# Performance work log

Measured on AMD Instinct MI355X. Metric: run time of the kernel, lower is better.

## Reference

```python
import jax, jax.numpy as jnp
import numpy as np

N = 20000   # nodes
E = 320000  # edges
F0 = 32     # num_features
H = 8       # GAT heads
G = 64      # graphs in batch


def setup_inputs() -> dict:
    key = jax.random.key(0)
    ks = jax.random.split(key, 16)
    def p(k, shape, s=0.05):
        return jax.random.normal(k, shape, jnp.float32) * s
    d = {}
    d['x'] = jax.random.normal(ks[0], (N, F0), jnp.float32)
    d['edge_index'] = jax.random.randint(ks[1], (2, E), 0, N, dtype=jnp.int32)
    d['edge_weights'] = jax.random.uniform(ks[2], (E,), jnp.float32)
    d['batch'] = jnp.sort(jax.random.randint(ks[3], (N,), 0, G, dtype=jnp.int32))
    # GATConv(32 -> 32, heads=8)
    d['W_gat'] = p(ks[4], (F0, H * F0)); d['att_src'] = p(ks[5], (H, F0))
    d['att_dst'] = p(ks[6], (H, F0));    d['b_gat'] = jnp.zeros((H * F0,), jnp.float32)
    # residual Linear(256 -> 1024) (widened so the residual add is shape-consistent)
    d['W_res'] = p(ks[7], (H * F0, 1024)); d['b_res'] = jnp.zeros((1024,), jnp.float32)
    # GCNConv(256 -> 512) + BN1
    d['W2'] = p(ks[8], (H * F0, 512)); d['b2'] = jnp.zeros((512,), jnp.float32)
    d['g1'] = jnp.ones((512,), jnp.float32); d['be1'] = jnp.zeros((512,), jnp.float32)
    d['m1'] = jnp.zeros((512,), jnp.float32); d['v1'] = jnp.ones((512,), jnp.float32)
    # GCNConv(512 -> 1024) + BN2
    d['W3'] = p(ks[9], (512, 1024)); d['b3'] = jnp.zeros((1024,), jnp.float32)
    d['g2'] = jnp.ones((1024,), jnp.float32); d['be2'] = jnp.zeros((1024,), jnp.float32)
    d['m2'] = jnp.zeros((1024,), jnp.float32); d['v2'] = jnp.ones((1024,), jnp.float32)
    # head
    d['Wf1'] = p(ks[10], (1024, 256)); d['bf1'] = jnp.zeros((256,), jnp.float32)
    d['Wf2'] = p(ks[11], (256, 2));    d['bf2'] = jnp.zeros((2,), jnp.float32)
    return d


def _add_self_loops(edge_index, edge_weight, n):
    loop = jnp.arange(n, dtype=edge_index.dtype)
    ei = jnp.concatenate([edge_index, jnp.stack([loop, loop])], axis=1)
    ew = jnp.concatenate([edge_weight, jnp.ones((n,), edge_weight.dtype)])
    return ei, ew


def _gat(x, edge_index, W, att_src, att_dst, b, n):
    # PyG GATConv, concat=True, eval (attention dropout off). Self-loops already added.
    src, dst = edge_index[0], edge_index[1]
    h = (x @ W).reshape(n, H, -1)                    # [N,H,C]
    a_s = jnp.einsum('nhc,hc->nh', h, att_src)        # [N,H]
    a_d = jnp.einsum('nhc,hc->nh', h, att_dst)
    e = jax.nn.leaky_relu(a_s[src] + a_d[dst], 0.2)   # [E,H]
    m = jax.ops.segment_max(e, dst, num_segments=n)   # softmax over incoming edges
    ex = jnp.exp(e - m[dst])
    s = jax.ops.segment_sum(ex, dst, num_segments=n)
    alpha = ex / s[dst]
    out = jax.ops.segment_sum(h[src] * alpha[:, :, None], dst, num_segments=n)
    return out.reshape(n, -1) + b                     # [N,H*C]


def _gcn(x, edge_index, w, W, b, n):
    # PyG GCNConv with symmetric normalization; self-loops (weight 1) already added.
    src, dst = edge_index[0], edge_index[1]
    deg = jax.ops.segment_sum(w, dst, num_segments=n)
    dinv = jnp.where(deg > 0, jax.lax.rsqrt(jnp.maximum(deg, 1e-12)), 0.0)
    norm = dinv[src] * w * dinv[dst]                  # [E]
    h = x @ W                                         # transform first (cheaper)
    return jax.ops.segment_sum(h[src] * norm[:, None], dst, num_segments=n) + b


def _bn(x, g, b, m, v):
    return g * (x - m) * jax.lax.rsqrt(v + 1e-5) + b


def reference(x, edge_index, edge_weights, batch, W_gat, att_src, att_dst, b_gat,
              W_res, b_res, W2, b2, g1, be1, m1, v1, W3, b3, g2, be2, m2, v2,
              Wf1, bf1, Wf2, bf2):
    n = x.shape[0]
    ei, ew = _add_self_loops(edge_index, edge_weights, n)
    h = jax.nn.relu(_gat(x, ei, W_gat, att_src, att_dst, b_gat, n))   # [N,256]
    res = h @ W_res + b_res                                           # [N,1024]
    h = _gcn(h, ei, ew, W2, b2, n)                                    # [N,512]
    h = jax.nn.relu(_bn(h, g1, be1, m1, v1))
    h = _gcn(h, ei, ew, W3, b3, n)                                    # [N,1024]
    h = jax.nn.relu(_bn(h, g2, be2, m2, v2))
    h = h + res
    pooled = jax.ops.segment_max(h, batch, num_segments=G)            # global max pool [G,1024]
    z = jax.nn.relu(pooled @ Wf1 + bf1)                               # dropout is eval no-op
    return z @ Wf2 + bf2                                              # [G,2]
```

## Files before the change

### kernel.cpp

```cpp
#include <hip/hip_runtime.h>
#include <hip/hip_bf16.h>
#include <hip/hip_fp8.h>

#define NN 20000
#define EE 320000
#define GG 64
#define EN (EE + NN)
#define MT 157
#define SB 79

typedef float f32x4 __attribute__((ext_vector_type(4)));
typedef __bf16 bf16x4 __attribute__((ext_vector_type(4)));
typedef __bf16 bf16x8 __attribute__((ext_vector_type(8)));

__device__ __forceinline__ void gl_lds16(const void* g, void* l) {
    __builtin_amdgcn_global_load_lds((const __attribute__((address_space(1))) void*)g,
                                     (__attribute__((address_space(3))) void*)l, 16, 0, 0);
}

__global__ void sentinel_kernel(float* out, int n) {
    int i = blockIdx.x * 256 + threadIdx.x;
    if (i < n) out[i] = 12345.0f;
}

__global__ __launch_bounds__(256) void front_kernel(
    const float* __restrict__ W2, const float* __restrict__ W3, const float* __restrict__ Wres,
    __bf16* __restrict__ W2t, __bf16* __restrict__ W3t, __bf16* __restrict__ Wrt,
    const float* __restrict__ x, const float* __restrict__ W_gat,
    const float* __restrict__ att_s, const float* __restrict__ att_d,
    float* __restrict__ a_s, float* __restrict__ a_d,
    const int* __restrict__ ei, const float* __restrict__ ew,
    int* deg_cnt, float* deg_w, float* __restrict__ pooled,
    __bf16* __restrict__ xb)
{
    __shared__ float smemf[4160];
    int b = blockIdx.x, tid = threadIdx.x;
    if (b < 224) {
        const float* W; __bf16* Wt; int K, N, bx, by;
        if (b < 32)       { W = W2;   Wt = W2t; K = 256; N = 512;  int bb = b;       bx = bb & 7;  by = bb >> 3; }
        else if (b < 160) { W = W3;   Wt = W3t; K = 512; N = 1024; int bb = b - 32;  bx = bb & 15; by = bb >> 4; }
        else              { W = Wres; Wt = Wrt; K = 256; N = 1024; int bb = b - 160; bx = bb & 15; by = bb >> 4; }
        int kb = by * 64, nb = bx * 64;
        int tx = tid & 63, ty = tid >> 6;
#pragma unroll
        for (int i = ty; i < 64; i += 4)
            smemf[i * 65 + tx] = W[(size_t)(kb + i) * N + nb + tx];
        __syncthreads();
#pragma unroll
        for (int i = ty; i < 64; i += 4)
            Wt[(size_t)(nb + i) * K + kb + tx] = (__bf16)smemf[tx * 65 + i];
    } else if (b < 352) {
        int bb = b - 224;
        float* wss = smemf;
        float* wsd = smemf + 256;
        float* xs  = smemf + 512;
        {
            int h = tid >> 5, k = tid & 31;
            float s = 0.f, d = 0.f;
#pragma unroll
            for (int c = 0; c < 32; c++) {
                float wv = W_gat[k * 256 + h * 32 + c];
                s += wv * att_s[h * 32 + c];
                d += wv * att_d[h * 32 + c];
            }
            wss[h * 32 + k] = s; wsd[h * 32 + k] = d;
        }
        __syncthreads();
        for (int n0 = bb * 32; n0 < NN; n0 += 128 * 32) {
#pragma unroll
            for (int i = 0; i < 4; i++) {
                int idx = tid + i * 256;
                xs[(idx >> 5) * 33 + (idx & 31)] = x[(size_t)n0 * 32 + idx];
            }
            __syncthreads();
            int nl = tid >> 3, h = tid & 7;
            float s = 0.f, d = 0.f;
#pragma unroll
            for (int k = 0; k < 32; k++) {
                float xv = xs[nl * 33 + k];
                s += xv * wss[h * 32 + k];
                d += xv * wsd[h * 32 + k];
            }
            a_s[(n0 + nl) * 8 + h] = s;
            a_d[(n0 + nl) * 8 + h] = d;
            __syncthreads();
        }
    } else if (b < 608) {
        int i = (b - 352) * 256 + tid;
        pooled[i] = -INFINITY;
    } else if (b < 1858) {
        int e = (b - 608) * 256 + tid;
        if (e < EE) {
            int dst = ei[EE + e];
            atomicAdd(&deg_cnt[dst], 1);
            atomicAdd(&deg_w[dst], ew[e]);
        }
    } else {
        int idx0 = (b - 1858) * 2048 + tid * 8;
        if (idx0 < NN * 32) {
            f32x4 a = *(const f32x4*)(x + idx0);
            f32x4 c = *(const f32x4*)(x + idx0 + 4);
            bf16x8 o;
#pragma unroll
            for (int u = 0; u < 4; u++) { o[u] = (__bf16)a[u]; o[u + 4] = (__bf16)c[u]; }
            *(bf16x8*)(xb + idx0) = o;
        }
    }
}

__global__ __launch_bounds__(256) void scan_blocks(const int* __restrict__ deg_cnt, int* __restrict__ bsum) {
    __shared__ int red[256];
    int tid = threadIdx.x, i = blockIdx.x * 256 + tid;
    red[tid] = (i < NN) ? deg_cnt[i] + 1 : 0;
    __syncthreads();
    for (int s = 128; s > 0; s >>= 1) { if (tid < s) red[tid] += red[tid + s]; __syncthreads(); }
    if (tid == 0) bsum[blockIdx.x] = red[0];
}

__global__ __launch_bounds__(256) void scan_write(const int* __restrict__ deg_cnt,
                                                  const int* __restrict__ bsum, int* __restrict__ rowptr) {
    __shared__ int sc[256];
    __shared__ int red[256];
    int tid = threadIdx.x, b = blockIdx.x, i = b * 256 + tid;
    red[tid] = (tid < b && tid < SB) ? bsum[tid] : 0;
    __syncthreads();
    for (int s = 128; s > 0; s >>= 1) { if (tid < s) red[tid] += red[tid + s]; __syncthreads(); }
    int boff = red[0];
    __syncthreads();
    int v = (i < NN) ? deg_cnt[i] + 1 : 0;
    sc[tid] = v;
    __syncthreads();
    for (int ofs = 1; ofs < 256; ofs <<= 1) {
        int t = (tid >= ofs) ? sc[tid - ofs] : 0;
        __syncthreads();
        sc[tid] += t;
        __syncthreads();
    }
    if (i < NN) rowptr[i] = boff + sc[tid] - v;
    if (b == SB - 1 && tid == 255) rowptr[NN] = boff + sc[255];
}

__global__ void fill_kernel(const int* __restrict__ ei, const float* __restrict__ ew,
                            const float* __restrict__ deg_w, const int* __restrict__ rowptr,
                            int* fill, int2* __restrict__ csre) {
    int e = blockIdx.x * 256 + threadIdx.x;
    if (e >= EN) return;
    int src, dst; float w;
    if (e < EE) { src = ei[e]; dst = ei[EE + e]; w = ew[e]; }
    else        { src = dst = e - EE; w = 1.0f; }
    int pos = atomicAdd(&fill[dst], 1);
    int slot = rowptr[dst] + pos;
    float norm = rsqrtf(deg_w[src] + 1.0f) * w * rsqrtf(deg_w[dst] + 1.0f);
    csre[slot] = make_int2(src, __float_as_int(norm));
}

__global__ __launch_bounds__(256) void gat_agg_x(
    const int* __restrict__ rowptr, const int2* __restrict__ csre,
    const float* __restrict__ a_s, const float* __restrict__ a_d,
    const __bf16* __restrict__ xb, __bf16* __restrict__ xagg)
{
    int widx = threadIdx.x >> 6, lane = threadIdx.x & 63;
    int node = blockIdx.x * 4 + widx;
    int base = rowptr[node], deg = rowptr[node + 1] - base;
    int hA = lane & 7, eslot = lane >> 3;
    int c = lane & 31, half = lane >> 5;
    float adA = a_d[node * 8 + hA];
    float acc0[4] = {}, acc1[4] = {}, acc2[4] = {}, acc3[4] = {};

    if (deg <= 64) {
        int sv = (lane < deg) ? csre[base + lane].x : 0;
        float ev[8];
        float psum = 0.f;
#pragma unroll
        for (int j = 0; j < 8; j++) {
            int e = j * 8 + eslot;
            float v = 0.f;
            if (e < deg) {
                int src = __shfl(sv, e);
                float t = a_s[src * 8 + hA] + adA;
                t = (t > 0.f) ? t : 0.2f * t;
                v = __expf(t);
            }
            ev[j] = v;
            psum += v;
        }
#pragma unroll
        for (int m = 8; m <= 32; m <<= 1) psum += __shfl_xor(psum, m);
        float sinv[4];
#pragma unroll
        for (int jj = 0; jj < 4; jj++) sinv[jj] = 1.f / __shfl(psum, half * 4 + jj);
#pragma unroll
        for (int j = 0; j < 8; j++) {
            if (j * 8 >= deg) break;
            int lim = min(8, deg - j * 8);
            int t = 0;
            for (; t + 3 < lim; t += 4) {
                int sA = __shfl(sv, j * 8 + t),     sB = __shfl(sv, j * 8 + t + 1);
                int sC = __shfl(sv, j * 8 + t + 2), sD = __shfl(sv, j * 8 + t + 3);
                float xvA = (float)xb[(size_t)sA * 32 + c];
                float xvB = (float)xb[(size_t)sB * 32 + c];
                float xvC = (float)xb[(size_t)sC * 32 + c];
                float xvD = (float)xb[(size_t)sD * 32 + c];
#pragma unroll
                for (int jj = 0; jj < 4; jj++) {
                    int hb = half * 4 + jj;
                    acc0[jj] += __shfl(ev[j], (t << 3) | hb) * sinv[jj] * xvA;
                    acc1[jj] += __shfl(ev[j], ((t + 1) << 3) | hb) * sinv[jj] * xvB;
                    acc2[jj] += __shfl(ev[j], ((t + 2) << 3) | hb) * sinv[jj] * xvC;
                    acc3[jj] += __shfl(ev[j], ((t + 3) << 3) | hb) * sinv[jj] * xvD;
                }
            }
            for (; t < lim; t++) {
                int src = __shfl(sv, j * 8 + t);
                float xv = (float)xb[(size_t)src * 32 + c];
#pragma unroll
                for (int jj = 0; jj < 4; jj++) {
                    float a = __shfl(ev[j], (t << 3) | (half * 4 + jj)) * sinv[jj];
                    acc0[jj] += a * xv;
                }
            }
        }
    } else {
        float sum = 0.f;
        for (int e = 0; e < deg; e++) {
            int src = csre[base + e].x;
            float t = a_s[src * 8 + hA] + adA;
            t = (t > 0.f) ? t : 0.2f * t;
            sum += __expf(t);
        }
        float sinv[4], ad4[4];
#pragma unroll
        for (int jj = 0; jj < 4; jj++) {
            sinv[jj] = 1.f / __shfl(sum, half * 4 + jj);
            ad4[jj] = a_d[node * 8 + half * 4 + jj];
        }
        for (int e = 0; e < deg; e++) {
            int src = csre[base + e].x;
            float xv = (float)xb[(size_t)src * 32 + c];
#pragma unroll
            for (int jj = 0; jj < 4; jj++) {
                float t = a_s[src * 8 + half * 4 + jj] + ad4[jj];
                t = (t > 0.f) ? t : 0.2f * t;
                acc0[jj] += __expf(t) * sinv[jj] * xv;
            }
        }
    }
#pragma unroll
    for (int jj = 0; jj < 4; jj++)
        xagg[(size_t)node * 256 + (half * 4 + jj) * 32 + c] =
            (__bf16)((acc0[jj] + acc1[jj]) + (acc2[jj] + acc3[jj]));
}

__global__ __launch_bounds__(256) void gat_post(
    const __bf16* __restrict__ xagg, const float* __restrict__ W,
    const float* __restrict__ b_gat, __bf16* __restrict__ h1,
    unsigned char* __restrict__ h1f)
{
    __shared__ float Ws[32 * 256];
    int tid = threadIdx.x;
#pragma unroll
    for (int k = 0; k < 32; k++) Ws[k * 256 + tid] = W[k * 256 + tid];
    float bg = b_gat[tid];
    int lbase = tid & 32;
    __syncthreads();
    for (int n = blockIdx.x; n < NN; n += gridDim.x) {
        float xv = (float)xagg[(size_t)n * 256 + tid];
        float acc = 0.f;
#pragma unroll
        for (int k = 0; k < 32; k++) acc += __shfl(xv, lbase + k) * Ws[k * 256 + tid];
        float v = fmaxf(acc + bg, 0.f);
        h1[(size_t)n * 256 + tid] = (__bf16)v;
        *reinterpret_cast<__hip_fp8_e4m3*>(&h1f[(size_t)n * 256 + tid]) = __hip_fp8_e4m3(16.0f * v);
    }
}

template <int C>
__global__ __launch_bounds__(256) void gcn_agg_fp8(
    const int* __restrict__ rowptr, const int2* __restrict__ csre,
    const unsigned char* __restrict__ feat, __bf16* __restrict__ out)
{
    constexpr int VB = C / 64;
    typedef __bf16 bf16v __attribute__((ext_vector_type(VB)));
    __shared__ float lut[256];
    int tid = threadIdx.x;
    {
        unsigned char bb = (unsigned char)tid;
        __hip_fp8_e4m3 q = *reinterpret_cast<__hip_fp8_e4m3*>(&bb);
        lut[tid] = ((float)q) * 0.0625f;
    }
    __syncthreads();
    int widx = tid >> 6, lane = tid & 63;
    int node = blockIdx.x * 4 + widx;
    int coff = lane * VB;
    int base = rowptr[node], deg = rowptr[node + 1] - base;
    float acc0[VB] = {}, acc1[VB] = {}, acc2[VB] = {}, acc3[VB] = {};
    const unsigned char* fb = feat + coff;
    auto ldv = [&](int src) -> unsigned long long {
        if constexpr (VB == 8) return *(const unsigned long long*)(fb + (size_t)src * C);
        else                   return (unsigned long long)(*(const unsigned int*)(fb + (size_t)src * C));
    };
    for (int e0 = 0; e0 < deg; e0 += 64) {
        int cnt = min(64, deg - e0);
        int sv = 0; float wv = 0.f;
        if (lane < cnt) { int2 m = csre[base + e0 + lane]; sv = m.x; wv = __int_as_float(m.y); }
        int s = 0;
        for (; s + 3 < cnt; s += 4) {
            int sA = __shfl(sv, s),     sB = __shfl(sv, s + 1);
            int sC = __shfl(sv, s + 2), sD = __shfl(sv, s + 3);
            float wA = __shfl(wv, s),     wB = __shfl(wv, s + 1);
            float wC = __shfl(wv, s + 2), wD = __shfl(wv, s + 3);
            unsigned long long vA = ldv(sA), vB = ldv(sB), vC = ldv(sC), vD = ldv(sD);
#pragma unroll
            for (int j = 0; j < VB; j++) {
                acc0[j] += wA * lut[(vA >> (8 * j)) & 0xff];
                acc1[j] += wB * lut[(vB >> (8 * j)) & 0xff];
                acc2[j] += wC * lut[(vC >> (8 * j)) & 0xff];
                acc3[j] += wD * lut[(vD >> (8 * j)) & 0xff];
            }
        }
        for (; s < cnt; s++) {
            int src = __shfl(sv, s);
            float w = __shfl(wv, s);
            unsigned long long v = ldv(src);
#pragma unroll
            for (int j = 0; j < VB; j++) acc0[j] += w * lut[(v >> (8 * j)) & 0xff];
        }
    }
    bf16v o;
#pragma unroll
    for (int j = 0; j < VB; j++) o[j] = (__bf16)((acc0[j] + acc1[j]) + (acc2[j] + acc3[j]));
    *(bf16v*)(out + (size_t)node * C + coff) = o;
}


__device__ __forceinline__ void stage_async64(
    const __bf16* __restrict__ A, int K, const __bf16* __restrict__ Wt,
    int bm, int bn, int k0, int tid, __bf16* As, __bf16* Bs)
{
#pragma unroll
    for (int i = 0; i < 2; i++) {
        int j = i * 512 + tid;
        int r = j >> 3, c = j & 7;
        const __bf16* gp = A + (size_t)(bm + r) * K + k0 + ((c ^ (r & 7)) * 8);
        gl_lds16(gp, As + (size_t)(j & ~63) * 8);
    }
#pragma unroll
    for (int i = 0; i < 2; i++) {
        int j = i * 512 + tid;
        int r = j >> 3, c = j & 7;
        const __bf16* gp = Wt + (size_t)(bn + r) * K + k0 + ((c ^ (r & 7)) * 8);
        gl_lds16(gp, Bs + (size_t)(j & ~63) * 8);
    }
}

__device__ __forceinline__ void mfma_step64(
    const __bf16* As, const __bf16* Bs, int wr, int wc, int l16, int q, f32x4 (&acc)[4][2])
{
#pragma unroll
    for (int ks = 0; ks < 2; ks++) {
        bf16x8 af[4], bfv[2];
#pragma unroll
        for (int mt = 0; mt < 4; mt++) {
            int row = wr * 64 + mt * 16 + l16;
            af[mt] = *(const bf16x8*)(As + row * 64 + (((ks * 4 + q) ^ (row & 7)) * 8));
        }
#pragma unroll
        for (int nt = 0; nt < 2; nt++) {
            int row = wc * 32 + nt * 16 + l16;
            bfv[nt] = *(const bf16x8*)(Bs + row * 64 + (((ks * 4 + q) ^ (row & 7)) * 8));
        }
#pragma unroll
        for (int mt = 0; mt < 4; mt++)
#pragma unroll
            for (int nt = 0; nt < 2; nt++)
                acc[mt][nt] = __builtin_amdgcn_mfma_f32_16x16x32_bf16(af[mt], bfv[nt], acc[mt][nt], 0, 0, 0);
    }
}

__device__ __forceinline__ void gemm_loop(
    const __bf16* __restrict__ A, int K, const __bf16* __restrict__ Wt,
    int bm, int bn, int tid, int wr, int wc, int l16, int q,
    __bf16* As, __bf16* Bs, f32x4 (&acc)[4][2])
{
    for (int k0 = 0; k0 < K; k0 += 64) {
        stage_async64(A, K, Wt, bm, bn, k0, tid, As, Bs);
        __syncthreads();
        mfma_step64(As, Bs, wr, wc, l16, q, acc);
        __syncthreads();
    }
}

__global__ __launch_bounds__(512) void gemm_bn_relu(
    const __bf16* __restrict__ A, const __bf16* __restrict__ Wt,
    int M, int K, int Nc,
    const float* __restrict__ bias,
    const float* __restrict__ g, const float* __restrict__ be,
    const float* __restrict__ mu, const float* __restrict__ var,
    unsigned char* __restrict__ C)
{
    __shared__ __bf16 As[128 * 64];
    __shared__ __bf16 Bs[128 * 64];
    int tid = threadIdx.x;
    int w = tid >> 6, wr = w >> 2, wc = w & 3;
    int l = tid & 63, q = l >> 4, l16 = l & 15;
    int i = blockIdx.x;
    int k = (i & 3) * MT + (i >> 2);
    int bm = (k >> 2) * 128, bn = (k & 3) * 128;
    f32x4 acc[4][2] = {};
    gemm_loop(A, K, Wt, bm, bn, tid, wr, wc, l16, q, As, Bs, acc);
#pragma unroll
    for (int nt = 0; nt < 2; nt++) {
        int gn = bn + wc * 32 + nt * 16 + l16;
        float s = g[gn] * rsqrtf(var[gn] + 1e-5f);
        float t = be[gn] - mu[gn] * s;
        float bv = bias[gn];
#pragma unroll
        for (int mt = 0; mt < 4; mt++)
#pragma unroll
            for (int r = 0; r < 4; r++) {
                int gm = bm + wr * 64 + mt * 16 + q * 4 + r;
                if (gm < M) {
                    float val = fmaxf((acc[mt][nt][r] + bv) * s + t, 0.f);
                    *reinterpret_cast<__hip_fp8_e4m3*>(&C[(size_t)gm * Nc + gn]) =
                        __hip_fp8_e4m3(16.0f * val);
                }
            }
    }
}

__device__ __forceinline__ void atomicMaxFloat(float* addr, float value) {
    if (value >= 0.f) atomicMax((int*)addr, __float_as_int(value));
    else              atomicMin((unsigned int*)addr, __float_as_uint(value));
}

__global__ __launch_bounds__(512) void gemm_final(
    const __bf16* __restrict__ A1, const __bf16* __restrict__ W3t,
    const __bf16* __restrict__ A2, const __bf16* __restrict__ Wrt,
    const float* __restrict__ b3, const float* __restrict__ bres,
    const float* __restrict__ g, const float* __restrict__ be,
    const float* __restrict__ mu, const float* __restrict__ var,
    const int* __restrict__ batch, float* __restrict__ pooled)
{
    const int M = NN;
    __shared__ __bf16 As[128 * 64];
    __shared__ __bf16 Bs[128 * 64];
    __shared__ int bat[128];
    int tid = threadIdx.x;
    int w = tid >> 6, wr = w >> 2, wc = w & 3;
    int l = tid & 63, q = l >> 4, l16 = l & 15;
    int i = blockIdx.x;
    int k = (i & 7) * MT + (i >> 3);
    int bm = (k >> 3) * 128, bn = (k & 7) * 128;
    if (tid < 128) bat[tid] = (bm + tid < M) ? batch[bm + tid] : -1;
    f32x4 acc[4][2] = {};
    f32x4 accR[4][2] = {};
    gemm_loop(A1, 512, W3t, bm, bn, tid, wr, wc, l16, q, As, Bs, acc);
    gemm_loop(A2, 256, Wrt, bm, bn, tid, wr, wc, l16, q, As, Bs, accR);
#pragma unroll
    for (int nt = 0; nt < 2; nt++) {
        int gn = bn + wc * 32 + nt * 16 + l16;
        float s = g[gn] * rsqrtf(var[gn] + 1e-5f);
        float t = be[gn] - mu[gn] * s;
        float bv3 = b3[gn];
        float bvr = bres[gn];
        int cb = -1; float run = 0.f;
#pragma unroll
        for (int mt = 0; mt < 4; mt++)
#pragma unroll
            for (int r = 0; r < 4; r++) {
                int lr = wr * 64 + mt * 16 + q * 4 + r;
                int id = bat[lr];
                if (id < 0) continue;
                float v = fmaxf((acc[mt][nt][r] + bv3) * s + t, 0.f) + accR[mt][nt][r] + bvr;
                if (id == cb) run = fmaxf(run, v);
                else {
                    if (cb >= 0) atomicMaxFloat(&pooled[cb * 1024 + gn], run);
                    cb = id; run = v;
                }
            }
        if (cb >= 0) atomicMaxFloat(&pooled[cb * 1024 + gn], run);
    }
}

__global__ void head_kernel(
    const float* __restrict__ pooled, const float* __restrict__ Wf1, const float* __restrict__ bf1,
    const float* __restrict__ Wf2, const float* __restrict__ bf2, float* __restrict__ out)
{
    int gph = blockIdx.x, tid = threadIdx.x;
    __shared__ float prow[1024];
    __shared__ float zred[256];
    for (int i = tid; i < 1024; i += 256) prow[i] = pooled[gph * 1024 + i];
    __syncthreads();
    float z = 0.f;
    for (int k = 0; k < 1024; k++) z += prow[k] * Wf1[k * 256 + tid];
    z = fmaxf(z + bf1[tid], 0.f);
    for (int c = 0; c < 2; c++) {
        zred[tid] = z * Wf2[tid * 2 + c];
        __syncthreads();
        for (int s = 128; s > 0; s >>= 1) { if (tid < s) zred[tid] += zred[tid + s]; __syncthreads(); }
        if (tid == 0) out[gph * 2 + c] = zred[0] + bf2[c];
        __syncthreads();
    }
}

extern "C" void kernel_launch(void* const* d_in, const int* in_sizes, int n_in,
                              void* d_out, int out_size, void* d_ws, size_t ws_size,
                              hipStream_t stream) {
    const float* x       = (const float*)d_in[0];
    const int*   ei      = (const int*)d_in[1];
    const float* ew      = (const float*)d_in[2];
    const int*   batch   = (const int*)d_in[3];
    const float* W_gat   = (const float*)d_in[4];
    const float* att_src = (const float*)d_in[5];
    const float* att_dst = (const float*)d_in[6];
    const float* b_gat   = (const float*)d_in[7];
    const float* W_res   = (const float*)d_in[8];
    const float* b_res   = (const float*)d_in[9];
    const float* W2      = (const float*)d_in[10];
    const float* b2v     = (const float*)d_in[11];
    const float* g1      = (const float*)d_in[12];
    const float* be1     = (const float*)d_in[13];
    const float* m1      = (const float*)d_in[14];
    const float* v1      = (const float*)d_in[15];
    const float* W3      = (const float*)d_in[16];
    const float* b3      = (const float*)d_in[17];
    const float* g2      = (const float*)d_in[18];
    const float* be2     = (const float*)d_in[19];
    const float* m2      = (const float*)d_in[20];
    const float* v2      = (const float*)d_in[21];
    const float* Wf1     = (const float*)d_in[22];
    const float* bf1     = (const float*)d_in[23];
    const float* Wf2     = (const float*)d_in[24];
    const float* bf2v    = (const float*)d_in[25];
    float* out           = (float*)d_out;

    char* ws = (char*)d_ws;
    size_t off = 0;
    auto alloc = [&](size_t bytes) { size_t o = off; off += (bytes + 255) & ~(size_t)255; return o; };
    size_t o_hlin   = alloc((size_t)NN * 256 * 2);
    size_t o_h1     = alloc((size_t)NN * 256 * 2);
    size_t o_h1f    = alloc((size_t)NN * 256);
    size_t o_h2     = alloc((size_t)NN * 512);
    size_t o_agg2   = alloc((size_t)NN * 512 * 2);
    size_t o_xb     = alloc((size_t)NN * 32 * 2);
    size_t o_as     = alloc((size_t)NN * 8 * 4);
    size_t o_ad     = alloc((size_t)NN * 8 * 4);
    size_t o_degc   = alloc((size_t)NN * 4);
    size_t o_degw   = alloc((size_t)NN * 4);
    size_t o_fill   = alloc((size_t)NN * 4);
    size_t o_rowptr = alloc((size_t)(NN + 1) * 4);
    size_t o_bsum   = alloc((size_t)SB * 4);
    size_t o_csre   = alloc((size_t)EN * 8);
    size_t o_pool   = alloc((size_t)GG * 1024 * 4);
    size_t o_w2t    = alloc((size_t)512 * 256 * 2);
    size_t o_w3t    = alloc((size_t)1024 * 512 * 2);
    size_t o_wrt    = alloc((size_t)1024 * 256 * 2);
    if (off > ws_size) {
        sentinel_kernel<<<(out_size + 255) / 256, 256, 0, stream>>>(out, out_size);
        return;
    }

    __bf16* xagg   = (__bf16*)(ws + o_hlin);
    __bf16* agg1   = xagg;
    __bf16* h1     = (__bf16*)(ws + o_h1);
    unsigned char* h1f = (unsigned char*)(ws + o_h1f);
    unsigned char* h2f = (unsigned char*)(ws + o_h2);
    __bf16* agg2   = (__bf16*)(ws + o_agg2);
    __bf16* xb     = (__bf16*)(ws + o_xb);
    float*  a_s    = (float*)(ws + o_as);
    float*  a_d    = (float*)(ws + o_ad);
    int*    degc   = (int*)(ws + o_degc);
    float*  degw   = (float*)(ws + o_degw);
    int*    fillb  = (int*)(ws + o_fill);
    int*    rowptr = (int*)(ws + o_rowptr);
    int*    bsum   = (int*)(ws + o_bsum);
    int2*   csre   = (int2*)(ws + o_csre);
    float*  pooled = (float*)(ws + o_pool);
    __bf16* W2t    = (__bf16*)(ws + o_w2t);
    __bf16* W3t    = (__bf16*)(ws + o_w3t);
    __bf16* Wrt    = (__bf16*)(ws + o_wrt);

    hipMemsetAsync(ws + o_degc, 0, o_rowptr - o_degc, stream);
    front_kernel<<<2171, 256, 0, stream>>>(W2, W3, W_res, W2t, W3t, Wrt,
        x, W_gat, att_src, att_dst, a_s, a_d, ei, ew, degc, degw, pooled, xb);

    scan_blocks<<<SB, 256, 0, stream>>>(degc, bsum);
    scan_write<<<SB, 256, 0, stream>>>(degc, bsum, rowptr);
    fill_kernel<<<(EN + 255) / 256, 256, 0, stream>>>(ei, ew, degw, rowptr, fillb, csre);

    gat_agg_x<<<NN / 4, 256, 0, stream>>>(rowptr, csre, a_s, a_d, xb, xagg);
    gat_post<<<1280, 256, 0, stream>>>(xagg, W_gat, b_gat, h1, h1f);

    gcn_agg_fp8<256><<<NN / 4, 256, 0, stream>>>(rowptr, csre, h1f, agg1);
    gemm_bn_relu<<<4 * MT, 512, 0, stream>>>(agg1, W2t, NN, 256, 512, b2v,
        g1, be1, m1, v1, h2f);
    gcn_agg_fp8<512><<<NN / 4, 256, 0, stream>>>(rowptr, csre, h2f, agg2);
    gemm_final<<<8 * MT, 512, 0, stream>>>(agg2, W3t, h1, Wrt,
        b3, b_res, g2, be2, m2, v2, batch, pooled);

    head_kernel<<<GG, 256, 0, stream>>>(pooled, Wf1, bf1, Wf2, bf2v, out);
}
```

Before: 376.2 us.

## Pack CSR edges into 32-bit words and process two nodes per wave in GCN aggregation

CSR edge entries are compressed from an int2 (source index plus fp32 norm) to one 32-bit word holding a 16-bit source index and an fp16 norm, halving edge-list traffic. The GCN aggregation kernel now maps half a wave (32 lanes) per node with wider per-lane loads, so each block covers 8 nodes. GAT aggregation pre-scales the attention weights by the softmax denominator once instead of multiplying inside the inner loop. Risks include lower norm precision, a 16-bit source index that relies on N fitting in 65536, and divergence when the two nodes sharing a wave have unequal degree.

```diff
diff --git a/kernel.cpp b/kernel.cpp
--- a/kernel.cpp
+++ b/kernel.cpp
@@ -1,6 +1,7 @@
 #include <hip/hip_runtime.h>
 #include <hip/hip_bf16.h>
 #include <hip/hip_fp8.h>
+#include <hip/hip_fp16.h>
 
 #define NN 20000
 #define EE 320000
@@ -142,7 +143,7 @@
 
 __global__ void fill_kernel(const int* __restrict__ ei, const float* __restrict__ ew,
                             const float* __restrict__ deg_w, const int* __restrict__ rowptr,
-                            int* fill, int2* __restrict__ csre) {
+                            int* fill, unsigned int* __restrict__ csru) {
     int e = blockIdx.x * 256 + threadIdx.x;
     if (e >= EN) return;
     int src, dst; float w;
@@ -151,11 +152,12 @@
     int pos = atomicAdd(&fill[dst], 1);
     int slot = rowptr[dst] + pos;
     float norm = rsqrtf(deg_w[src] + 1.0f) * w * rsqrtf(deg_w[dst] + 1.0f);
-    csre[slot] = make_int2(src, __float_as_int(norm));
+    unsigned short hb = __half_as_ushort(__float2half(norm));
+    csru[slot] = (unsigned int)src | ((unsigned int)hb << 16);
 }
 
 __global__ __launch_bounds__(256) void gat_agg_x(
-    const int* __restrict__ rowptr, const int2* __restrict__ csre,
+    const int* __restrict__ rowptr, const unsigned int* __restrict__ csru,
     const float* __restrict__ a_s, const float* __restrict__ a_d,
     const __bf16* __restrict__ xb, __bf16* __restrict__ xagg)
 {
@@ -168,7 +170,7 @@
     float acc0[4] = {}, acc1[4] = {}, acc2[4] = {}, acc3[4] = {};
 
     if (deg <= 64) {
-        int sv = (lane < deg) ? csre[base + lane].x : 0;
+        int sv = (lane < deg) ? (int)(csru[base + lane] & 0xffffu) : 0;
         float ev[8];
         float psum = 0.f;
 #pragma unroll
@@ -186,9 +188,9 @@
         }
 #pragma unroll
         for (int m = 8; m <= 32; m <<= 1) psum += __shfl_xor(psum, m);
-        float sinv[4];
-#pragma unroll
-        for (int jj = 0; jj < 4; jj++) sinv[jj] = 1.f / __shfl(psum, half * 4 + jj);
+        float sinv_own = 1.f / psum;
+#pragma unroll
+        for (int j = 0; j < 8; j++) ev[j] *= sinv_own;
 #pragma unroll
         for (int j = 0; j < 8; j++) {
             if (j * 8 >= deg) break;
@@ -204,10 +206,10 @@
 #pragma unroll
                 for (int jj = 0; jj < 4; jj++) {
                     int hb = half * 4 + jj;
-                    acc0[jj] += __shfl(ev[j], (t << 3) | hb) * sinv[jj] * xvA;
-                    acc1[jj] += __shfl(ev[j], ((t + 1) << 3) | hb) * sinv[jj] * xvB;
-                    acc2[jj] += __shfl(ev[j], ((t + 2) << 3) | hb) * sinv[jj] * xvC;
-                    acc3[jj] += __shfl(ev[j], ((t + 3) << 3) | hb) * sinv[jj] * xvD;
+                    acc0[jj] += __shfl(ev[j], (t << 3) | hb) * xvA;
+                    acc1[jj] += __shfl(ev[j], ((t + 1) << 3) | hb) * xvB;
+                    acc2[jj] += __shfl(ev[j], ((t + 2) << 3) | hb) * xvC;
+                    acc3[jj] += __shfl(ev[j], ((t + 3) << 3) | hb) * xvD;
                 }
             }
             for (; t < lim; t++) {
@@ -215,7 +217,7 @@
                 float xv = (float)xb[(size_t)src * 32 + c];
 #pragma unroll
                 for (int jj = 0; jj < 4; jj++) {
-                    float a = __shfl(ev[j], (t << 3) | (half * 4 + jj)) * sinv[jj];
+                    float a = __shfl(ev[j], (t << 3) | (half * 4 + jj));
                     acc0[jj] += a * xv;
                 }
             }
@@ -223,7 +225,7 @@
     } else {
         float sum = 0.f;
         for (int e = 0; e < deg; e++) {
-            int src = csre[base + e].x;
+            int src = (int)(csru[base + e] & 0xffffu);
             float t = a_s[src * 8 + hA] + adA;
             t = (t > 0.f) ? t : 0.2f * t;
             sum += __expf(t);
@@ -235,7 +237,7 @@
             ad4[jj] = a_d[node * 8 + half * 4 + jj];
         }
         for (int e = 0; e < deg; e++) {
-            int src = csre[base + e].x;
+            int src = (int)(csru[base + e] & 0xffffu);
             float xv = (float)xb[(size_t)src * 32 + c];
 #pragma unroll
             for (int jj = 0; jj < 4; jj++) {
@@ -276,10 +278,11 @@
 
 template <int C>
 __global__ __launch_bounds__(256) void gcn_agg_fp8(
-    const int* __restrict__ rowptr, const int2* __restrict__ csre,
+    const int* __restrict__ rowptr, const unsigned int* __restrict__ csru,
     const unsigned char* __restrict__ feat, __bf16* __restrict__ out)
 {
-    constexpr int VB = C / 64;
+    constexpr int VB = C / 32;
+    constexpr int NW = VB / 8;
     typedef __bf16 bf16v __attribute__((ext_vector_type(VB)));
     __shared__ float lut[256];
     int tid = threadIdx.x;
@@ -289,47 +292,49 @@
         lut[tid] = ((float)q) * 0.0625f;
     }
     __syncthreads();
-    int widx = tid >> 6, lane = tid & 63;
-    int node = blockIdx.x * 4 + widx;
-    int coff = lane * VB;
+    int wave = tid >> 6, lane = tid & 63;
+    int g = lane >> 5, l = lane & 31, gb = g << 5;
+    int node = blockIdx.x * 8 + wave * 2 + g;
     int base = rowptr[node], deg = rowptr[node + 1] - base;
-    float acc0[VB] = {}, acc1[VB] = {}, acc2[VB] = {}, acc3[VB] = {};
-    const unsigned char* fb = feat + coff;
-    auto ldv = [&](int src) -> unsigned long long {
-        if constexpr (VB == 8) return *(const unsigned long long*)(fb + (size_t)src * C);
-        else                   return (unsigned long long)(*(const unsigned int*)(fb + (size_t)src * C));
+    int degmax = max(deg, __shfl(deg, lane ^ 32));
+    float acc[VB] = {};
+    const unsigned char* fb = feat + l * VB;
+
+    auto ldrow = [&](unsigned int m, unsigned long long* v) {
+        const unsigned char* p = fb + (size_t)(m & 0xffffu) * C;
+        if constexpr (NW == 2) { ulonglong2 t = *(const ulonglong2*)p; v[0] = t.x; v[1] = t.y; }
+        else                   { v[0] = *(const unsigned long long*)p; }
     };
-    for (int e0 = 0; e0 < deg; e0 += 64) {
-        int cnt = min(64, deg - e0);
-        int sv = 0; float wv = 0.f;
-        if (lane < cnt) { int2 m = csre[base + e0 + lane]; sv = m.x; wv = __int_as_float(m.y); }
+    auto accrow = [&](unsigned int m, const unsigned long long* v) {
+        float w = __half2float(__ushort_as_half((unsigned short)(m >> 16)));
+#pragma unroll
+        for (int q = 0; q < NW; q++)
+#pragma unroll
+            for (int j = 0; j < 8; j++)
+                acc[q * 8 + j] += w * lut[(v[q] >> (8 * j)) & 0xff];
+    };
+
+    for (int e0 = 0; e0 < degmax; e0 += 32) {
+        unsigned int mv = (e0 + l < deg) ? csru[base + e0 + l] : 0u;
+        int cnt = min(32, degmax - e0);
         int s = 0;
         for (; s + 3 < cnt; s += 4) {
-            int sA = __shfl(sv, s),     sB = __shfl(sv, s + 1);
-            int sC = __shfl(sv, s + 2), sD = __shfl(sv, s + 3);
-            float wA = __shfl(wv, s),     wB = __shfl(wv, s + 1);
-            float wC = __shfl(wv, s + 2), wD = __shfl(wv, s + 3);
-            unsigned long long vA = ldv(sA), vB = ldv(sB), vC = ldv(sC), vD = ldv(sD);
-#pragma unroll
-            for (int j = 0; j < VB; j++) {
-                acc0[j] += wA * lut[(vA >> (8 * j)) & 0xff];
-                acc1[j] += wB * lut[(vB >> (8 * j)) & 0xff];
-                acc2[j] += wC * lut[(vC >> (8 * j)) & 0xff];
-                acc3[j] += wD * lut[(vD >> (8 * j)) & 0xff];
-            }
+            unsigned int mA = __shfl(mv, gb + s),     mB = __shfl(mv, gb + s + 1);
+            unsigned int mC = __shfl(mv, gb + s + 2), mD = __shfl(mv, gb + s + 3);
+            unsigned long long vA[NW], vB[NW], vC[NW], vD[NW];
+            ldrow(mA, vA); ldrow(mB, vB); ldrow(mC, vC); ldrow(mD, vD);
+            accrow(mA, vA); accrow(mB, vB); accrow(mC, vC); accrow(mD, vD);
         }
         for (; s < cnt; s++) {
-            int src = __shfl(sv, s);
-            float w = __shfl(wv, s);
-            unsigned long long v = ldv(src);
-#pragma unroll
-            for (int j = 0; j < VB; j++) acc0[j] += w * lut[(v >> (8 * j)) & 0xff];
+            unsigned int m = __shfl(mv, gb + s);
+            unsigned long long v[NW];
+            ldrow(m, v); accrow(m, v);
         }
     }
     bf16v o;
 #pragma unroll
-    for (int j = 0; j < VB; j++) o[j] = (__bf16)((acc0[j] + acc1[j]) + (acc2[j] + acc3[j]));
-    *(bf16v*)(out + (size_t)node * C + coff) = o;
+    for (int j = 0; j < VB; j++) o[j] = (__bf16)acc[j];
+    *(bf16v*)(out + (size_t)node * C + l * VB) = o;
 }
 
 
@@ -550,7 +555,7 @@
     size_t o_fill   = alloc((size_t)NN * 4);
     size_t o_rowptr = alloc((size_t)(NN + 1) * 4);
     size_t o_bsum   = alloc((size_t)SB * 4);
-    size_t o_csre   = alloc((size_t)EN * 8);
+    size_t o_csre   = alloc((size_t)EN * 4);
     size_t o_pool   = alloc((size_t)GG * 1024 * 4);
     size_t o_w2t    = alloc((size_t)512 * 256 * 2);
     size_t o_w3t    = alloc((size_t)1024 * 512 * 2);
@@ -574,7 +579,7 @@
     int*    fillb  = (int*)(ws + o_fill);
     int*    rowptr = (int*)(ws + o_rowptr);
     int*    bsum   = (int*)(ws + o_bsum);
-    int2*   csre   = (int2*)(ws + o_csre);
+    unsigned int* csru = (unsigned int*)(ws + o_csre);
     float*  pooled = (float*)(ws + o_pool);
     __bf16* W2t    = (__bf16*)(ws + o_w2t);
     __bf16* W3t    = (__bf16*)(ws + o_w3t);
@@ -586,15 +591,15 @@
 
     scan_blocks<<<SB, 256, 0, stream>>>(degc, bsum);
     scan_write<<<SB, 256, 0, stream>>>(degc, bsum, rowptr);
-    fill_kernel<<<(EN + 255) / 256, 256, 0, stream>>>(ei, ew, degw, rowptr, fillb, csre);
-
-    gat_agg_x<<<NN / 4, 256, 0, stream>>>(rowptr, csre, a_s, a_d, xb, xagg);
+    fill_kernel<<<(EN + 255) / 256, 256, 0, stream>>>(ei, ew, degw, rowptr, fillb, csru);
+
+    gat_agg_x<<<NN / 4, 256, 0, stream>>>(rowptr, csru, a_s, a_d, xb, xagg);
     gat_post<<<1280, 256, 0, stream>>>(xagg, W_gat, b_gat, h1, h1f);
 
-    gcn_agg_fp8<256><<<NN / 4, 256, 0, stream>>>(rowptr, csre, h1f, agg1);
+    gcn_agg_fp8<256><<<NN / 8, 256, 0, stream>>>(rowptr, csru, h1f, agg1);
     gemm_bn_relu<<<4 * MT, 512, 0, stream>>>(agg1, W2t, NN, 256, 512, b2v,
         g1, be1, m1, v1, h2f);
-    gcn_agg_fp8<512><<<NN / 4, 256, 0, stream>>>(rowptr, csre, h2f, agg2);
+    gcn_agg_fp8<512><<<NN / 8, 256, 0, stream>>>(rowptr, csru, h2f, agg2);
     gemm_final<<<8 * MT, 512, 0, stream>>>(agg2, W3t, h1, Wrt,
         b3, b_res, g2, be2, m2, v2, batch, pooled);
 
```

Result: slower. 389.7 us (+3.6%).
